# Performance work log

Measured on AMD Instinct MI355X. Metric: run time of the kernel, lower is better.

## Reference

```python
import jax, jax.numpy as jnp
import numpy as np

SEQ_LEN = 720
PRED_LEN = 720
ENC_IN = 862
PCA_RANK = 32
CUT_FREQ = 48
LENGTH_RATIO = (SEQ_LEN + PRED_LEN) / SEQ_LEN  # 2.0
FREQ_OUT = int(CUT_FREQ * LENGTH_RATIO)        # 96
B = 256


def setup_inputs() -> dict:
    key = jax.random.key(0)
    ks = jax.random.split(key, 7)
    return {
        "x_enc": jax.random.normal(ks[0], (B, SEQ_LEN, ENC_IN), dtype=jnp.float32),
        "pca_encode": jax.random.normal(ks[1], (ENC_IN, PCA_RANK), dtype=jnp.float32),
        "pca_decode": jax.random.normal(ks[2], (PCA_RANK, ENC_IN), dtype=jnp.float32),
        "Wr": jax.random.normal(ks[3], (PCA_RANK, FREQ_OUT, CUT_FREQ), dtype=jnp.float32) * 0.1,
        "Wi": jax.random.normal(ks[4], (PCA_RANK, FREQ_OUT, CUT_FREQ), dtype=jnp.float32) * 0.1,
        "br": jax.random.normal(ks[5], (PCA_RANK, FREQ_OUT), dtype=jnp.float32) * 0.1,
        "bi": jax.random.normal(ks[6], (PCA_RANK, FREQ_OUT), dtype=jnp.float32) * 0.1,
    }


def reference(x_enc, pca_encode, pca_decode, Wr, Wi, br, bi):
    # PCA compress: [B, T, C] @ [C, R] -> [B, T, R]
    x = x_enc @ pca_encode
    # Instance normalization over time (torch.var default is unbiased, ddof=1)
    x_mean = x.mean(axis=1, keepdims=True)
    x = x - x_mean
    x_var = jnp.var(x, axis=1, keepdims=True, ddof=1)
    x_std = jnp.sqrt(x_var + 1e-5)
    x = x / x_std
    # Frequency-domain linear, batched over the R channels as one complex GEMM
    x_freq_low = jnp.fft.rfft(x, axis=1)[:, :CUT_FREQ, :]        # [B, F, R] complex
    W = (Wr + 1j * Wi).astype(jnp.complex64)                     # [R, G, F]
    b = (br + 1j * bi).astype(jnp.complex64)                     # [R, G]
    out_freq = jnp.einsum('bfr,rgf->bgr', x_freq_low, W) + b.T[None]  # [B, G, R]
    # Inverse FFT to the extended length, rescale, take prediction horizon
    out = jnp.fft.irfft(out_freq, n=SEQ_LEN + PRED_LEN, axis=1) * LENGTH_RATIO
    out = out[:, -PRED_LEN:, :]
    # De-normalize and PCA decompress
    out = out * x_std + x_mean
    return out @ pca_decode  # [B, pred_len, C]
```

## Files before the change

kernel.cpp:

```cpp
#include <hip/hip_runtime.h>
#include <math.h>

#define B_SZ   256
#define T_SEQ  720
#define C_INN  862
#define RANK   32
#define FCUT   48
#define GOUT   96
#define KTILES 27

#define WMR_OFF    (0)
#define WMI_OFF    (147456)
#define PARTF_OFF  (294912)
#define PARTG_OFF  (2654208)
#define STATSG_OFF (2703360)
#define OBG_OFF    (2719744)
#define PSWZ_OFF   (5898240)
#define FTABB_OFF  (5912064)
#define ITABB_OFF  (5947392)
#define DSWZ_OFF   (6016512)

typedef __attribute__((ext_vector_type(8))) short bf16x8;
typedef __attribute__((ext_vector_type(4))) float f32x4;

__device__ inline short f2bf(float f) {
    union { float f; unsigned u; } v; v.f = f;
    unsigned r = (v.u + 0x7fffu + ((v.u >> 16) & 1u)) >> 16;
    return (short)r;
}
__device__ inline unsigned pkhi(float lo, float hi) {
    return __builtin_amdgcn_perm(__float_as_uint(hi), __float_as_uint(lo), 0x07060302u);
}
union U8 { bf16x8 v; unsigned u[4]; };

__global__ __launch_bounds__(256) void k_prep(const float* __restrict__ P,
                                              const float* __restrict__ D,
                                              const float* __restrict__ Wr,
                                              const float* __restrict__ Wi,
                                              short* __restrict__ Pswz,
                                              short* __restrict__ ftabB,
                                              short* __restrict__ itabB,
                                              short* __restrict__ Dswz,
                                              float4* __restrict__ WmR,
                                              float4* __restrict__ WmI) {
    int idx = blockIdx.x * 256 + threadIdx.x;
    const float TWO_PI = 6.28318530717958647692f;
    if (idx < 138240) {
        int i = idx & 7, l = (idx >> 3) & 63, rest = idx >> 9;
        int ks = rest % 6, mt = rest / 6;
        int t = mt * 16 + (l & 15);
        int k = ks * 32 + ((l >> 4) << 3) + i;
        int g = k >> 1, odd = k & 1;
        float val;
        if (g == 0) {
            val = odd ? 0.0f : 0.5f;
        } else {
            int m = (g * (720 + t)) % 1440;
            float th = TWO_PI * (float)m * (1.0f / 1440.0f);
            val = odd ? sinf(th) : cosf(th);
        }
        itabB[idx] = f2bf(val);
    } else if (idx < 138240 + 70656) {
        int j = idx - 138240;
        int i = j & 7, l = (j >> 3) & 63, rest = j >> 9;
        int ks = rest % 23, mt = rest / 23;
        int row = mt * 16 + (l & 15);
        int t = ks * 32 + ((l >> 4) << 3) + i;
        int f = row >> 1, odd = row & 1;
        float val = 0.0f;
        if (t < T_SEQ) {
            int m = (f * t) % T_SEQ;
            float th = TWO_PI * (float)m * (1.0f / 720.0f);
            val = odd ? -sinf(th) : cosf(th);
        }
        ftabB[j] = f2bf(val);
    } else if (idx < 138240 + 70656 + 27648) {
        int j = idx - 138240 - 70656;
        int i = j & 7, lane = (j >> 3) & 63, rest = j >> 9;
        int ct = rest & 1, kt = rest >> 1;
        int k = kt * 32 + ((lane >> 4) << 3) + i;
        int c = ct * 16 + (lane & 15);
        float v = (k < C_INN) ? P[k * RANK + c] : 0.0f;
        Pswz[j] = f2bf(v);
    } else if (idx < 264192) {
        int j = idx - 138240 - 70656 - 27648;
        int i = j & 7, lane = (j >> 3) & 63, ct = j >> 9;
        int k = ((lane >> 4) << 3) + i;
        int c = ct * 16 + (lane & 15);
        float v = (c < C_INN) ? D[k * C_INN + c] : 0.0f;
        Dswz[j] = f2bf(v);
    } else {
        int j = idx - 264192;
        int r = j & 31;
        int q = (j >> 5) % 12;
        int g = (j >> 5) / 12;
        size_t src = ((size_t)(r * 96 + g)) * 48 + q * 4;
        WmR[(g * 12 + q) * 32 + r] = *(const float4*)(Wr + src);
        WmI[(g * 12 + q) * 32 + r] = *(const float4*)(Wi + src);
    }
}

__global__ __launch_bounds__(512) void k_encode(const float* __restrict__ x,
                                                const short* __restrict__ Pswz,
                                                const short* __restrict__ ftabB,
                                                float* __restrict__ partF,
                                                float* __restrict__ partg) {
    __shared__ short YbL[8192];
    __shared__ float red[512];
    int bid = blockIdx.x;
    int b = bid / 3, seg = bid % 3;
    int tid = threadIdx.x, l = tid & 63, w = tid >> 6;
    int h = l >> 4, c0 = l & 15, c1 = c0 + 16;
    const float* xb = x + (size_t)b * T_SEQ * C_INN;
    const bf16x8* pb = (const bf16x8*)Pswz;

    int mtbase = seg * 16;
    int ksbase = seg * 8;
    int nks    = (seg < 2) ? 8 : 7;
    int mt0 = mtbase + w;
    int mt1 = mtbase + 8 + w;
    bool valid1 = (seg < 2) || (w < 5);
    const float* xr0 = xb + (size_t)(mt0 * 16 + c0) * C_INN;
    const float* xr1 = valid1 ? (xb + (size_t)(mt1 * 16 + c0) * C_INN) : xr0;

    if (seg == 2 && tid < 128) {
        int ct = tid >> 6;
        int lp = 32 + ((tid >> 1) & 31);
        int half = tid & 1;
        short4 z; z.x = 0; z.y = 0; z.z = 0; z.w = 0;
        *(short4*)&YbL[((6 * 2 + ct) * 64 + lp) * 8 + half * 4] = z;
    }

    f32x4 acc00 = {0,0,0,0}, acc01 = {0,0,0,0};
    f32x4 acc10 = {0,0,0,0}, acc11 = {0,0,0,0};

#pragma unroll 2
    for (int kt = 0; kt < KTILES - 1; ++kt) {
        int kbase = kt * 32 + h * 8;
        float4 u00 = *(const float4*)(xr0 + kbase);
        float4 u01 = *(const float4*)(xr0 + kbase + 4);
        float4 u10 = *(const float4*)(xr1 + kbase);
        float4 u11 = *(const float4*)(xr1 + kbase + 4);
        bf16x8 b0 = pb[(kt * 2 + 0) * 64 + l];
        bf16x8 b1 = pb[(kt * 2 + 1) * 64 + l];
        U8 A0, A1;
        A0.u[0] = pkhi(u00.x, u00.y); A0.u[1] = pkhi(u00.z, u00.w);
        A0.u[2] = pkhi(u01.x, u01.y); A0.u[3] = pkhi(u01.z, u01.w);
        A1.u[0] = pkhi(u10.x, u10.y); A1.u[1] = pkhi(u10.z, u10.w);
        A1.u[2] = pkhi(u11.x, u11.y); A1.u[3] = pkhi(u11.z, u11.w);
        acc00 = __builtin_amdgcn_mfma_f32_16x16x32_bf16(A0.v, b0, acc00, 0, 0, 0);
        acc01 = __builtin_amdgcn_mfma_f32_16x16x32_bf16(A0.v, b1, acc01, 0, 0, 0);
        acc10 = __builtin_amdgcn_mfma_f32_16x16x32_bf16(A1.v, b0, acc10, 0, 0, 0);
        acc11 = __builtin_amdgcn_mfma_f32_16x16x32_bf16(A1.v, b1, acc11, 0, 0, 0);
    }
    {
        int kbase = 832 + h * 8;
        bf16x8 b0 = pb[(26 * 2 + 0) * 64 + l];
        bf16x8 b1 = pb[(26 * 2 + 1) * 64 + l];
        const float* xrs[2] = {xr0, xr1};
        f32x4* accs[2][2] = {{&acc00,&acc01},{&acc10,&acc11}};
#pragma unroll
        for (int tt = 0; tt < 2; ++tt) {
            const float* xr = xrs[tt];
            float vals[8];
            float2 u0 = *(const float2*)(xr + kbase);
            float2 u1 = *(const float2*)(xr + kbase + 2);
            float2 u2 = *(const float2*)(xr + kbase + 4);
            vals[0] = u0.x; vals[1] = u0.y;
            vals[2] = u1.x; vals[3] = u1.y;
            vals[4] = u2.x; vals[5] = u2.y;
            if (h < 3) {
                float2 u3 = *(const float2*)(xr + kbase + 6);
                vals[6] = u3.x; vals[7] = u3.y;
            } else {
                vals[6] = 0.f; vals[7] = 0.f;
            }
            U8 A;
            A.u[0] = pkhi(vals[0], vals[1]); A.u[1] = pkhi(vals[2], vals[3]);
            A.u[2] = pkhi(vals[4], vals[5]); A.u[3] = pkhi(vals[6], vals[7]);
            *accs[tt][0] = __builtin_amdgcn_mfma_f32_16x16x32_bf16(A.v, b0, *accs[tt][0], 0, 0, 0);
            *accs[tt][1] = __builtin_amdgcn_mfma_f32_16x16x32_bf16(A.v, b1, *accs[tt][1], 0, 0, 0);
        }
    }

    {
        float s0 = 0.f, q0 = 0.f, s1 = 0.f, q1 = 0.f;
#pragma unroll
        for (int j = 0; j < 4; ++j) {
            float v;
            v = acc00[j]; s0 += v; q0 += v * v;
            v = acc01[j]; s1 += v; q1 += v * v;
            if (valid1) {
                v = acc10[j]; s0 += v; q0 += v * v;
                v = acc11[j]; s1 += v; q1 += v * v;
            }
        }
        s0 += __shfl_xor(s0, 16); s0 += __shfl_xor(s0, 32);
        q0 += __shfl_xor(q0, 16); q0 += __shfl_xor(q0, 32);
        s1 += __shfl_xor(s1, 16); s1 += __shfl_xor(s1, 32);
        q1 += __shfl_xor(q1, 16); q1 += __shfl_xor(q1, 32);
        if (l < 16) {
            red[c0 * 8 + w]       = s0;
            red[c1 * 8 + w]       = s1;
            red[256 + c0 * 8 + w] = q0;
            red[256 + c1 * 8 + w] = q1;
        }
    }
    __syncthreads();
    if (tid < 32) {
        float s = 0.f;
        for (int ww = 0; ww < 8; ++ww) s += red[tid * 8 + ww];
        partg[bid * 64 + tid] = s;
    } else if (tid < 64) {
        int c = tid - 32;
        float q = 0.f;
        for (int ww = 0; ww < 8; ++ww) q += red[256 + c * 8 + ww];
        partg[bid * 64 + tid] = q;
    }

    {
        int ibase = (h & 1) * 4;
#define WRTILEL(MT, A0v, A1v)                                                      \
        {                                                                          \
            int lp  = ((2 * (MT) + (h >> 1)) & 3) * 16 + c0;                       \
            int ksl = ((MT) >> 1) - ksbase;                                        \
            short4 w0, w1;                                                         \
            w0.x = f2bf(A0v[0]); w0.y = f2bf(A0v[1]);                              \
            w0.z = f2bf(A0v[2]); w0.w = f2bf(A0v[3]);                              \
            w1.x = f2bf(A1v[0]); w1.y = f2bf(A1v[1]);                              \
            w1.z = f2bf(A1v[2]); w1.w = f2bf(A1v[3]);                              \
            *(short4*)&YbL[((ksl * 2 + 0) * 64 + lp) * 8 + ibase] = w0;            \
            *(short4*)&YbL[((ksl * 2 + 1) * 64 + lp) * 8 + ibase] = w1;            \
        }
        WRTILEL(mt0, acc00, acc01);
        if (valid1) WRTILEL(mt1, acc10, acc11);
#undef WRTILEL
    }
    __syncthreads();

    {
        float* pf = partF + (size_t)bid * 3072;
        for (int idx = w; idx < 12; idx += 8) {
            int fmt = idx >> 1, fct = idx & 1;
            f32x4 acc = {0.f, 0.f, 0.f, 0.f};
            for (int ksl = 0; ksl < nks; ++ksl) {
                bf16x8 a  = ((const bf16x8*)ftabB)[(fmt * 23 + ksbase + ksl) * 64 + l];
                bf16x8 bb = *(const bf16x8*)&YbL[((ksl * 2 + fct) * 64 + l) * 8];
                acc = __builtin_amdgcn_mfma_f32_16x16x32_bf16(a, bb, acc, 0, 0, 0);
            }
#pragma unroll
            for (int j = 0; j < 4; ++j)
                pf[(fmt * 16 + h * 4 + j) * 32 + fct * 16 + c0] = acc[j];
        }
    }
}

__global__ __launch_bounds__(512) void k_front(const float* __restrict__ partF,
                                               const float* __restrict__ partg,
                                               float* __restrict__ statsg,
                                               const float4* __restrict__ WmR,
                                               const float4* __restrict__ WmI,
                                               const float* __restrict__ brr,
                                               const float* __restrict__ bii,
                                               short* __restrict__ OBg) {
    __shared__ float Fre[FCUT * 32];
    __shared__ float Fim[FCUT * 32];
    __shared__ float meanS[32], istdS[32];
    int b   = blockIdx.x;
    int tid = threadIdx.x;

    if (tid < 32) {
        const float* pg = partg + (size_t)b * 192;
        float s = pg[tid] + pg[64 + tid] + pg[128 + tid];
        float q = pg[32 + tid] + pg[96 + tid] + pg[160 + tid];
        float mean = s / 720.0f;
        float var  = (q - 720.0f * mean * mean) / 719.0f;
        float sd   = sqrtf(var + 1e-5f);
        meanS[tid] = mean;
        istdS[tid] = 1.0f / sd;
        statsg[b * 64 + tid]      = mean;
        statsg[b * 64 + 32 + tid] = sd;
    }
    __syncthreads();

    {
        const float* p0 = partF + (size_t)b * 3 * 3072;
        for (int e = tid; e < 3072; e += 512) {
            int row = e >> 5, r = e & 31;
            float v = p0[e] + p0[3072 + e] + p0[6144 + e];
            if (row == 0) v -= 720.0f * meanS[r];
            v *= istdS[r];
            int f = row >> 1;
            if (row & 1) Fim[f * 32 + r] = v;
            else         Fre[f * 32 + r] = v;
        }
    }
    __syncthreads();

    {
        int r = tid & 31, gg = tid >> 5;
        unsigned* OBb = (unsigned*)(OBg + (size_t)b * 6144);
        for (int g = gg; g < GOUT; g += 16) {
            float are = brr[r * GOUT + g];
            float aim = bii[r * GOUT + g];
            const float4* wr4 = WmR + (size_t)g * 384 + r;
            const float4* wi4 = WmI + (size_t)g * 384 + r;
#pragma unroll 3
            for (int q = 0; q < 12; ++q) {
                float4 wr = wr4[q * 32], wi = wi4[q * 32];
                int f0 = q * 4;
                float fr, fi;
                fr = Fre[(f0 + 0) * 32 + r]; fi = Fim[(f0 + 0) * 32 + r];
                are += fr * wr.x - fi * wi.x;  aim += fr * wi.x + fi * wr.x;
                fr = Fre[(f0 + 1) * 32 + r]; fi = Fim[(f0 + 1) * 32 + r];
                are += fr * wr.y - fi * wi.y;  aim += fr * wi.y + fi * wr.y;
                fr = Fre[(f0 + 2) * 32 + r]; fi = Fim[(f0 + 2) * 32 + r];
                are += fr * wr.z - fi * wi.z;  aim += fr * wi.z + fi * wr.z;
                fr = Fre[(f0 + 3) * 32 + r]; fi = Fim[(f0 + 3) * 32 + r];
                are += fr * wr.w - fi * wi.w;  aim += fr * wi.w + fi * wr.w;
            }
            int ks   = g >> 4;
            int kk   = (2 * g) & 31;
            int lane = (kk >> 3) * 16 + (r & 15);
            int ct   = r >> 4;
            unsigned lo = (unsigned short)f2bf(are);
            unsigned hi = (unsigned short)f2bf(-aim);
            OBb[((((ks * 2 + ct) * 64 + lane) * 8) + (kk & 7)) >> 1] = lo | (hi << 16);
        }
    }
}

__global__ __launch_bounds__(512) void k_dec(const short* __restrict__ OBg,
                                             const float* __restrict__ statsg,
                                             const short* __restrict__ itabB,
                                             const short* __restrict__ Dswz,
                                             float* __restrict__ out) {
    __shared__ short zfrag[15 * 512];
    __shared__ __align__(16) float stage[16 * 862];
    int bid = blockIdx.x;
    int b = bid / 3, seg = bid % 3;
    int tid = threadIdx.x, l = tid & 63, w = tid >> 6;
    int h = l >> 4, c0 = l & 15, c1 = c0 + 16;
    const bf16x8* ob = (const bf16x8*)(OBg + (size_t)b * 6144);
    const bf16x8* db = (const bf16x8*)Dswz;
    float* outb = out + (size_t)b * T_SEQ * C_INN;

    float mu0 = statsg[b * 64 + c0], sd0 = statsg[b * 64 + 32 + c0];
    float mu1 = statsg[b * 64 + c1], sd1 = statsg[b * 64 + 32 + c1];

    int lp0 = (c0 >> 3) * 16 + h * 4;
    int lp1 = (2 + (c0 >> 3)) * 16 + h * 4;

    for (int ti = w; ti < 15; ti += 8) {
        int mt = seg * 15 + ti;
        f32x4 A0 = {0.f, 0.f, 0.f, 0.f};
        f32x4 A1 = {0.f, 0.f, 0.f, 0.f};
#pragma unroll
        for (int ks = 0; ks < 6; ++ks) {
            bf16x8 a  = ((const bf16x8*)itabB)[(mt * 6 + ks) * 64 + l];
            bf16x8 b0 = ob[(ks * 2 + 0) * 64 + l];
            bf16x8 b1 = ob[(ks * 2 + 1) * 64 + l];
            A0 = __builtin_amdgcn_mfma_f32_16x16x32_bf16(a, b0, A0, 0, 0, 0);
            A1 = __builtin_amdgcn_mfma_f32_16x16x32_bf16(a, b1, A1, 0, 0, 0);
        }
        short* zf = zfrag + ti * 512;
#pragma unroll
        for (int j = 0; j < 4; ++j) {
            zf[(lp0 + j) * 8 + (l & 7)] = f2bf(A0[j] * (1.0f / 360.0f) * sd0 + mu0);
            zf[(lp1 + j) * 8 + (l & 7)] = f2bf(A1[j] * (1.0f / 360.0f) * sd1 + mu1);
        }
    }
    __syncthreads();

    for (int ti = 0; ti < 15; ++ti) {
        int mt = seg * 15 + ti;
        bf16x8 a = *(const bf16x8*)&zfrag[ti * 512 + l * 8];
        for (int ct = w; ct < 54; ct += 8) {
            bf16x8 bb = db[ct * 64 + l];
            f32x4 acc = {0.f, 0.f, 0.f, 0.f};
            acc = __builtin_amdgcn_mfma_f32_16x16x32_bf16(a, bb, acc, 0, 0, 0);
            int c = ct * 16 + c0;
            if (c < C_INN) {
#pragma unroll
                for (int j = 0; j < 4; ++j)
                    stage[(h * 4 + j) * C_INN + c] = acc[j];
            }
        }
        __syncthreads();
        float* dst = outb + (size_t)mt * 16 * C_INN;
        const float4* sg4 = (const float4*)stage;
        for (int f = tid; f < 3448; f += 512)
            *(float4*)(dst + f * 4) = sg4[f];
        __syncthreads();
    }
}

extern "C" void kernel_launch(void* const* d_in, const int* in_sizes, int n_in,
                              void* d_out, int out_size, void* d_ws, size_t ws_size,
                              hipStream_t stream) {
    const float* x   = (const float*)d_in[0];
    const float* P   = (const float*)d_in[1];
    const float* D   = (const float*)d_in[2];
    const float* Wr  = (const float*)d_in[3];
    const float* Wi  = (const float*)d_in[4];
    const float* brr = (const float*)d_in[5];
    const float* bii = (const float*)d_in[6];
    float* out = (float*)d_out;
    float* ws  = (float*)d_ws;

    float4* WmR   = (float4*)(ws + WMR_OFF);
    float4* WmI   = (float4*)(ws + WMI_OFF);
    float*  partF = ws + PARTF_OFF;
    float*  partg = ws + PARTG_OFF;
    float*  statsg= ws + STATSG_OFF;
    short*  OBg   = (short*)(ws + OBG_OFF);
    short*  Pswz  = (short*)(ws + PSWZ_OFF);
    short*  ftabB = (short*)(ws + FTABB_OFF);
    short*  itabB = (short*)(ws + ITABB_OFF);
    short*  Dswz  = (short*)(ws + DSWZ_OFF);

    k_prep<<<1176, 256, 0, stream>>>(P, D, Wr, Wi, Pswz, ftabB, itabB, Dswz, WmR, WmI);
    k_encode<<<768, 512, 0, stream>>>(x, Pswz, ftabB, partF, partg);
    k_front<<<B_SZ, 512, 0, stream>>>(partF, partg, statsg, WmR, WmI, brr, bii, OBg);
    k_dec<<<768, 512, 0, stream>>>(OBg, statsg, itabB, Dswz, out);
}
```

Measured before the change: 333.5 us.

## Fuse frequency-domain linear stage into decode kernel

Merges the per-batch normalization and complex frequency linear (former k_front) into k_dec, keeping stats and the bf16 OB operand in shared memory aliased onto the stage buffer. This removes one kernel launch and the global write/read of OBg and statsg. In exchange each batch's frequency linear is recomputed by all three segment blocks, adding redundant compute and weight reads per block.

Result: slower. 363.4 us (+9.0%).

```diff
diff --git a/kernel.cpp b/kernel.cpp
--- a/kernel.cpp
+++ b/kernel.cpp
@@ -13,8 +13,6 @@
 #define WMI_OFF    (147456)
 #define PARTF_OFF  (294912)
 #define PARTG_OFF  (2654208)
-#define STATSG_OFF (2703360)
-#define OBG_OFF    (2719744)
 #define PSWZ_OFF   (5898240)
 #define FTABB_OFF  (5912064)
 #define ITABB_OFF  (5947392)
@@ -255,19 +253,28 @@
     }
 }
 
-__global__ __launch_bounds__(512) void k_front(const float* __restrict__ partF,
-                                               const float* __restrict__ partg,
-                                               float* __restrict__ statsg,
-                                               const float4* __restrict__ WmR,
-                                               const float4* __restrict__ WmI,
-                                               const float* __restrict__ brr,
-                                               const float* __restrict__ bii,
-                                               short* __restrict__ OBg) {
-    __shared__ float Fre[FCUT * 32];
-    __shared__ float Fim[FCUT * 32];
-    __shared__ float meanS[32], istdS[32];
-    int b   = blockIdx.x;
-    int tid = threadIdx.x;
+__global__ __launch_bounds__(512) void k_dec(const float* __restrict__ partF,
+                                             const float* __restrict__ partg,
+                                             const float4* __restrict__ WmR,
+                                             const float4* __restrict__ WmI,
+                                             const float* __restrict__ brr,
+                                             const float* __restrict__ bii,
+                                             const short* __restrict__ itabB,
+                                             const short* __restrict__ Dswz,
+                                             float* __restrict__ out) {
+    __shared__ short zfrag[15 * 512];
+    __shared__ __align__(16) float stage[16 * 862];
+    __shared__ float meanS[32], stdS[32], istdS[32];
+    float* Fre = stage;
+    float* Fim = stage + 1536;
+    short* OBl = (short*)(stage + 3072);
+
+    int bid = blockIdx.x;
+    int b = bid / 3, seg = bid % 3;
+    int tid = threadIdx.x, l = tid & 63, w = tid >> 6;
+    int h = l >> 4, c0 = l & 15, c1 = c0 + 16;
+    const bf16x8* db = (const bf16x8*)Dswz;
+    float* outb = out + (size_t)b * T_SEQ * C_INN;
 
     if (tid < 32) {
         const float* pg = partg + (size_t)b * 192;
@@ -277,9 +284,8 @@
         float var  = (q - 720.0f * mean * mean) / 719.0f;
         float sd   = sqrtf(var + 1e-5f);
         meanS[tid] = mean;
+        stdS[tid]  = sd;
         istdS[tid] = 1.0f / sd;
-        statsg[b * 64 + tid]      = mean;
-        statsg[b * 64 + 32 + tid] = sd;
     }
     __syncthreads();
 
@@ -299,7 +305,7 @@
 
     {
         int r = tid & 31, gg = tid >> 5;
-        unsigned* OBb = (unsigned*)(OBg + (size_t)b * 6144);
+        unsigned* OBu = (unsigned*)OBl;
         for (int g = gg; g < GOUT; g += 16) {
             float are = brr[r * GOUT + g];
             float aim = bii[r * GOUT + g];
@@ -325,49 +331,36 @@
             int ct   = r >> 4;
             unsigned lo = (unsigned short)f2bf(are);
             unsigned hi = (unsigned short)f2bf(-aim);
-            OBb[((((ks * 2 + ct) * 64 + lane) * 8) + (kk & 7)) >> 1] = lo | (hi << 16);
-        }
-    }
-}
-
-__global__ __launch_bounds__(512) void k_dec(const short* __restrict__ OBg,
-                                             const float* __restrict__ statsg,
-                                             const short* __restrict__ itabB,
-                                             const short* __restrict__ Dswz,
-                                             float* __restrict__ out) {
-    __shared__ short zfrag[15 * 512];
-    __shared__ __align__(16) float stage[16 * 862];
-    int bid = blockIdx.x;
-    int b = bid / 3, seg = bid % 3;
-    int tid = threadIdx.x, l = tid & 63, w = tid >> 6;
-    int h = l >> 4, c0 = l & 15, c1 = c0 + 16;
-    const bf16x8* ob = (const bf16x8*)(OBg + (size_t)b * 6144);
-    const bf16x8* db = (const bf16x8*)Dswz;
-    float* outb = out + (size_t)b * T_SEQ * C_INN;
-
-    float mu0 = statsg[b * 64 + c0], sd0 = statsg[b * 64 + 32 + c0];
-    float mu1 = statsg[b * 64 + c1], sd1 = statsg[b * 64 + 32 + c1];
-
+            OBu[((((ks * 2 + ct) * 64 + lane) * 8) + (kk & 7)) >> 1] = lo | (hi << 16);
+        }
+    }
+    __syncthreads();
+
+    float mu0 = meanS[c0], sd0 = stdS[c0];
+    float mu1 = meanS[c1], sd1 = stdS[c1];
     int lp0 = (c0 >> 3) * 16 + h * 4;
     int lp1 = (2 + (c0 >> 3)) * 16 + h * 4;
 
-    for (int ti = w; ti < 15; ti += 8) {
-        int mt = seg * 15 + ti;
-        f32x4 A0 = {0.f, 0.f, 0.f, 0.f};
-        f32x4 A1 = {0.f, 0.f, 0.f, 0.f};
-#pragma unroll
-        for (int ks = 0; ks < 6; ++ks) {
-            bf16x8 a  = ((const bf16x8*)itabB)[(mt * 6 + ks) * 64 + l];
-            bf16x8 b0 = ob[(ks * 2 + 0) * 64 + l];
-            bf16x8 b1 = ob[(ks * 2 + 1) * 64 + l];
-            A0 = __builtin_amdgcn_mfma_f32_16x16x32_bf16(a, b0, A0, 0, 0, 0);
-            A1 = __builtin_amdgcn_mfma_f32_16x16x32_bf16(a, b1, A1, 0, 0, 0);
-        }
-        short* zf = zfrag + ti * 512;
-#pragma unroll
-        for (int j = 0; j < 4; ++j) {
-            zf[(lp0 + j) * 8 + (l & 7)] = f2bf(A0[j] * (1.0f / 360.0f) * sd0 + mu0);
-            zf[(lp1 + j) * 8 + (l & 7)] = f2bf(A1[j] * (1.0f / 360.0f) * sd1 + mu1);
+    {
+        const bf16x8* ob = (const bf16x8*)OBl;
+        for (int ti = w; ti < 15; ti += 8) {
+            int mt = seg * 15 + ti;
+            f32x4 A0 = {0.f, 0.f, 0.f, 0.f};
+            f32x4 A1 = {0.f, 0.f, 0.f, 0.f};
+#pragma unroll
+            for (int ks = 0; ks < 6; ++ks) {
+                bf16x8 a  = ((const bf16x8*)itabB)[(mt * 6 + ks) * 64 + l];
+                bf16x8 b0 = ob[(ks * 2 + 0) * 64 + l];
+                bf16x8 b1 = ob[(ks * 2 + 1) * 64 + l];
+                A0 = __builtin_amdgcn_mfma_f32_16x16x32_bf16(a, b0, A0, 0, 0, 0);
+                A1 = __builtin_amdgcn_mfma_f32_16x16x32_bf16(a, b1, A1, 0, 0, 0);
+            }
+            short* zf = zfrag + ti * 512;
+#pragma unroll
+            for (int j = 0; j < 4; ++j) {
+                zf[(lp0 + j) * 8 + (l & 7)] = f2bf(A0[j] * (1.0f / 360.0f) * sd0 + mu0);
+                zf[(lp1 + j) * 8 + (l & 7)] = f2bf(A1[j] * (1.0f / 360.0f) * sd1 + mu1);
+            }
         }
     }
     __syncthreads();
@@ -412,8 +405,6 @@
     float4* WmI   = (float4*)(ws + WMI_OFF);
     float*  partF = ws + PARTF_OFF;
     float*  partg = ws + PARTG_OFF;
-    float*  statsg= ws + STATSG_OFF;
-    short*  OBg   = (short*)(ws + OBG_OFF);
     short*  Pswz  = (short*)(ws + PSWZ_OFF);
     short*  ftabB = (short*)(ws + FTABB_OFF);
     short*  itabB = (short*)(ws + ITABB_OFF);
@@ -421,6 +412,5 @@
 
     k_prep<<<1176, 256, 0, stream>>>(P, D, Wr, Wi, Pswz, ftabB, itabB, Dswz, WmR, WmI);
     k_encode<<<768, 512, 0, stream>>>(x, Pswz, ftabB, partF, partg);
-    k_front<<<B_SZ, 512, 0, stream>>>(partF, partg, statsg, WmR, WmI, brr, bii, OBg);
-    k_dec<<<768, 512, 0, stream>>>(OBg, statsg, itabB, Dswz, out);
-}
+    k_dec<<<768, 512, 0, stream>>>(partF, partg, WmR, WmI, brr, bii, itabB, Dswz, out);
+}
```
